# Kernel tuning notes

Measured on AMD Instinct MI355X. Metric: run time of the kernel, lower is better.

## Reference

```python
import jax, jax.numpy as jnp
import numpy as np

EPS = 1e-5

def _bn(x, w, b, rm, rv):
    # eval-mode BatchNorm over channel axis (x: [..., C] broadcastable)
    return (x - rm) * (w * jax.lax.rsqrt(rv + EPS)) + b

def setup_inputs() -> dict:
    key = jax.random.key(0)
    ks = jax.random.split(key, 20)
    B, C, H, W = 2, 64, 96, 96
    Cq = C // 8  # query/key channels
    Cr = C // 8  # SE reduction channels
    s = 0.05
    inp = {
        'x': jax.random.normal(ks[0], (B, C, H, W), jnp.float32),
        'wq': jax.random.normal(ks[1], (Cq, C), jnp.float32) * s,
        'bq': jnp.zeros((Cq,), jnp.float32),
        'wk': jax.random.normal(ks[2], (Cq, C), jnp.float32) * s,
        'bk': jnp.zeros((Cq,), jnp.float32),
        'wv': jax.random.normal(ks[3], (C, C), jnp.float32) * s,
        'bv': jnp.zeros((C,), jnp.float32),
        'gamma': jnp.full((1,), 0.5, jnp.float32),
        'bn_w': jnp.ones((C,), jnp.float32),
        'bn_b': jnp.zeros((C,), jnp.float32),
        'bn_rm': jax.random.normal(ks[4], (C,), jnp.float32) * 0.1,
        'bn_rv': jax.random.uniform(ks[5], (C,), jnp.float32) + 0.5,
        'se_w1': jax.random.normal(ks[6], (Cr, C), jnp.float32) * s,
        'se_b1': jnp.zeros((Cr,), jnp.float32),
        'se_bn1_w': jnp.ones((Cr,), jnp.float32),
        'se_bn1_b': jnp.zeros((Cr,), jnp.float32),
        'se_bn1_rm': jax.random.normal(ks[7], (Cr,), jnp.float32) * 0.1,
        'se_bn1_rv': jax.random.uniform(ks[8], (Cr,), jnp.float32) + 0.5,
        'se_w2': jax.random.normal(ks[9], (C, Cr), jnp.float32) * s,
        'se_b2': jnp.zeros((C,), jnp.float32),
        'se_bn2_w': jnp.ones((C,), jnp.float32),
        'se_bn2_b': jnp.zeros((C,), jnp.float32),
        'se_bn2_rm': jax.random.normal(ks[10], (C,), jnp.float32) * 0.1,
        'se_bn2_rv': jax.random.uniform(ks[11], (C,), jnp.float32) + 0.5,
    }
    return inp

def reference(x, wq, bq, wk, bk, wv, bv, gamma, bn_w, bn_b, bn_rm, bn_rv,
              se_w1, se_b1, se_bn1_w, se_bn1_b, se_bn1_rm, se_bn1_rv,
              se_w2, se_b2, se_bn2_w, se_bn2_b, se_bn2_rm, se_bn2_rv):
    B, C, H, W = x.shape
    N = H * W
    xf = x.reshape(B, C, N)
    # PAM branch: 1x1 conv projections
    q = jnp.einsum('oc,bcn->bno', wq, xf) + bq            # [B,N,C/8]
    k = jnp.einsum('oc,bcn->bon', wk, xf) + bk[:, None]    # [B,C/8,N]
    v = jnp.einsum('oc,bcn->bon', wv, xf) + bv[:, None]    # [B,C,N]
    energy = jnp.einsum('bno,bom->bnm', q, k)              # [B,N,N]
    attn = jax.nn.softmax(energy, axis=-1)
    # out[b,c,i] = sum_j v[b,c,j] * attn[b,i,j]  (bmm(V, attn^T))
    out = jnp.einsum('bcj,bij->bci', v, attn)
    out = gamma[0] * out
    out = _bn(out, bn_w[:, None], bn_b[:, None], bn_rm[:, None], bn_rv[:, None])
    pam = out.reshape(B, C, H, W)
    # SE branch: GAP + 1x1 conv-bn-relu x2, multiplicative gate
    a = xf.mean(axis=2)                                    # [B,C]
    a1 = jax.nn.relu(_bn(a @ se_w1.T + se_b1, se_bn1_w, se_bn1_b, se_bn1_rm, se_bn1_rv))
    a2 = jax.nn.relu(_bn(a1 @ se_w2.T + se_b2, se_bn2_w, se_bn2_b, se_bn2_rm, se_bn2_rv))
    se = x * a2[:, :, None, None]
    return x + se + pam
```

## Files before the change

### kernel.cpp

```cpp
#include <hip/hip_runtime.h>
#include <hip/hip_bf16.h>

#define B_SZ   2
#define C_CH   64
#define NQ     8
#define QKS    16
#define NPIX   9216
#define NKS    576
#define QBLKS  288
#define KPART  4
#define KEYS_P 2304
#define NCHUNK 36
#define SM_F   2080
#define NP4    2304
#define KSTEP2 1024
#define VSTEP  4096

typedef short bf16x8 __attribute__((ext_vector_type(8)));
typedef float f32x4  __attribute__((ext_vector_type(4)));
typedef float f32x16 __attribute__((ext_vector_type(16)));
typedef unsigned u32x4 __attribute__((ext_vector_type(4)));
typedef unsigned uint2v __attribute__((ext_vector_type(2)));

static __device__ __forceinline__ unsigned pack2bf(float a, float b){
    unsigned r;
    asm("v_cvt_pk_bf16_f32 %0, %1, %2" : "=v"(r) : "v"(a), "v"(b));
    return r;
}

static __device__ __forceinline__ float exp2r(float x){
    return __builtin_amdgcn_exp2f(x);
}

__global__ __launch_bounds__(256) void prep_kernel(
    const float* __restrict__ x,
    const float* __restrict__ wq, const float* __restrict__ bq,
    const float* __restrict__ wk, const float* __restrict__ bk,
    const float* __restrict__ wv, const float* __restrict__ bv,
    __hip_bfloat16* __restrict__ qp, __hip_bfloat16* __restrict__ kp,
    __hip_bfloat16* __restrict__ vswz, float* __restrict__ amean)
{
    const int blk = blockIdx.x, tid = threadIdx.x;
    if (blk < 144){
        int t  = blk*256 + tid;
        int n  = (t % NP4) * 4;
        int c8 = (t / NP4) & 7;
        int b  = t / (NP4*8);
        c8 = __builtin_amdgcn_readfirstlane(c8);
        b  = __builtin_amdgcn_readfirstlane(b);
        float acc[8][4];
#pragma unroll
        for (int k = 0; k < 8; ++k){
            float bvv = bv[c8*8 + k];
            acc[k][0] = bvv; acc[k][1] = bvv; acc[k][2] = bvv; acc[k][3] = bvv;
        }
#pragma unroll 4
        for (int ci = 0; ci < C_CH; ++ci){
            const float4 xv = *reinterpret_cast<const float4*>(
                x + (size_t)(b*C_CH + ci)*NPIX + n);
#pragma unroll
            for (int k = 0; k < 8; ++k){
                float w = wv[(c8*8 + k)*C_CH + ci];
                acc[k][0] = fmaf(xv.x, w, acc[k][0]);
                acc[k][1] = fmaf(xv.y, w, acc[k][1]);
                acc[k][2] = fmaf(xv.z, w, acc[k][2]);
                acc[k][3] = fmaf(xv.w, w, acc[k][3]);
            }
        }
#pragma unroll
        for (int k = 0; k < 8; ++k){
            int c = c8*8 + k;
            size_t base = ((size_t)((b*NKS + (n >> 4))*2 + (c >> 5)))*512
                        + (((n >> 3) & 1) << 8) + ((c & 31) << 3) + (n & 7);
            unsigned long long wpk =
                (unsigned long long)pack2bf(acc[k][0], acc[k][1]) |
                ((unsigned long long)pack2bf(acc[k][2], acc[k][3]) << 32);
            *reinterpret_cast<unsigned long long*>(vswz + base) = wpk;
        }
    } else if (blk < 180){
        int t  = (blk - 144)*256 + tid;
        int n  = (t % NP4) * 4;
        int o8 = (t / NP4) & 1;
        int b  = t / (NP4*2);
        o8 = __builtin_amdgcn_readfirstlane(o8);
        b  = __builtin_amdgcn_readfirstlane(b);
        const bool isq = (o8 == 0);
        const float* w    = isq ? wq : wk;
        const float* bias = isq ? bq : bk;
        float acc[8][4];
#pragma unroll
        for (int k = 0; k < 8; ++k){
            float bb = bias[k];
            acc[k][0] = bb; acc[k][1] = bb; acc[k][2] = bb; acc[k][3] = bb;
        }
#pragma unroll 4
        for (int ci = 0; ci < C_CH; ++ci){
            const float4 xv = *reinterpret_cast<const float4*>(
                x + (size_t)(b*C_CH + ci)*NPIX + n);
#pragma unroll
            for (int k = 0; k < 8; ++k){
                float wv_ = w[k*C_CH + ci];
                acc[k][0] = fmaf(xv.x, wv_, acc[k][0]);
                acc[k][1] = fmaf(xv.y, wv_, acc[k][1]);
                acc[k][2] = fmaf(xv.z, wv_, acc[k][2]);
                acc[k][3] = fmaf(xv.w, wv_, acc[k][3]);
            }
        }
        if (isq){
#pragma unroll
            for (int k = 0; k < 8; ++k)
#pragma unroll
                for (int px = 0; px < 4; ++px) acc[k][px] *= 1.44269504f;
        }
        __hip_bfloat16* dst = isq ? qp : kp;
        u32x4 zr; zr[0] = 0; zr[1] = 0; zr[2] = 0; zr[3] = 0;
#pragma unroll
        for (int px = 0; px < 4; ++px){
            u32x4 row;
            row[0] = pack2bf(acc[0][px], acc[1][px]);
            row[1] = pack2bf(acc[2][px], acc[3][px]);
            row[2] = pack2bf(acc[4][px], acc[5][px]);
            row[3] = pack2bf(acc[6][px], acc[7][px]);
            __hip_bfloat16* d0 = dst + ((size_t)(b*NPIX + n + px))*QKS;
            *reinterpret_cast<u32x4*>(d0)     = row;
            *reinterpret_cast<u32x4*>(d0 + 8) = zr;
        }
    } else {
        int bc = blk - 180;
        float s = 0.f;
        for (int i = tid; i < NPIX; i += 256) s += x[(size_t)bc*NPIX + i];
#pragma unroll
        for (int o = 32; o > 0; o >>= 1) s += __shfl_down(s, o, 64);
        __shared__ float red[4];
        if ((tid & 63) == 0) red[tid >> 6] = s;
        __syncthreads();
        if (tid == 0) amean[bc] = (red[0] + red[1] + red[2] + red[3]) * (1.f / (float)NPIX);
    }
}

__global__ __launch_bounds__(256, 4) void flash_fused(
    const __hip_bfloat16* __restrict__ qp,
    const __hip_bfloat16* __restrict__ kp,
    const __hip_bfloat16* __restrict__ vswz,
    const float* __restrict__ amean,
    const float* __restrict__ sw1, const float* __restrict__ sb1,
    const float* __restrict__ s1w, const float* __restrict__ s1b,
    const float* __restrict__ s1m, const float* __restrict__ s1v,
    const float* __restrict__ sw2, const float* __restrict__ sb2,
    const float* __restrict__ s2w, const float* __restrict__ s2b,
    const float* __restrict__ s2m, const float* __restrict__ s2v,
    const float* __restrict__ x,
    const float* __restrict__ gamma,
    const float* __restrict__ bnw, const float* __restrict__ bnb,
    const float* __restrict__ bnm, const float* __restrict__ bnv,
    float* __restrict__ out)
{
    __shared__ __align__(16) float sm[4*SM_F];

    const int qt2 = blockIdx.x, b = blockIdx.y;
    const int p  = threadIdx.x >> 6;
    const int l  = threadIdx.x & 63;
    const int lc = l & 31;
    const int lh = l >> 5;

    bf16x8 qfrag = *reinterpret_cast<const bf16x8*>(
        qp + ((size_t)(b*NPIX + qt2*32 + lc))*QKS + lh*8);

    bf16x8 ones;
#pragma unroll
    for (int i = 0; i < 8; ++i) ones[i] = (short)0x3F80;

    f32x16 zero16;
#pragma unroll
    for (int i = 0; i < 16; ++i) zero16[i] = 0.f;

    f32x16 Of0 = zero16, Of1 = zero16;
    f32x16 Lacc = zero16;

    const __hip_bfloat16* kptr = kp + ((size_t)(b*NPIX + p*KEYS_P + lc))*QKS + lh*8;
    const __hip_bfloat16* vptr = vswz + ((size_t)((b*NKS + p*(KEYS_P/16))*2))*512 + l*8;

    auto CHUNK = [&](const bf16x8& k0, const bf16x8& k1){
        bf16x8 vf[8];
#pragma unroll
        for (int t = 0; t < 8; ++t)
            vf[t] = *reinterpret_cast<const bf16x8*>(vptr + t*512);
        vptr += VSTEP;

        unsigned D[16];
#pragma unroll
        for (int kt = 0; kt < 2; ++kt){
            f32x16 s = __builtin_amdgcn_mfma_f32_32x32x16_bf16(
                kt ? k1 : k0, qfrag, zero16, 0, 0, 0);
#pragma unroll
            for (int g = 0; g < 4; ++g){
                float e0 = exp2r(s[4*g+0]), e1 = exp2r(s[4*g+1]);
                float e2 = exp2r(s[4*g+2]), e3 = exp2r(s[4*g+3]);
                D[kt*8 + g*2 + 0] = pack2bf(e0, e1);
                D[kt*8 + g*2 + 1] = pack2bf(e2, e3);
            }
        }
#pragma unroll
        for (int ks = 0; ks < 4; ++ks){
            const int base = (ks >> 1)*8 + (ks & 1)*4;
            uint2v r0 = __builtin_amdgcn_permlane32_swap(D[base+0], D[base+2], false, false);
            uint2v r1 = __builtin_amdgcn_permlane32_swap(D[base+1], D[base+3], false, false);
            u32x4 pu; pu[0] = r0[0]; pu[1] = r1[0]; pu[2] = r0[1]; pu[3] = r1[1];
            bf16x8 pf = __builtin_bit_cast(bf16x8, pu);
            Of0  = __builtin_amdgcn_mfma_f32_32x32x16_bf16(vf[ks*2+0], pf, Of0, 0, 0, 0);
            Of1  = __builtin_amdgcn_mfma_f32_32x32x16_bf16(vf[ks*2+1], pf, Of1, 0, 0, 0);
            Lacc = __builtin_amdgcn_mfma_f32_32x32x16_bf16(ones,       pf, Lacc, 0, 0, 0);
        }
    };

    bf16x8 kA0 = *reinterpret_cast<const bf16x8*>(kptr);
    bf16x8 kA1 = *reinterpret_cast<const bf16x8*>(kptr + 512);
    kptr += KSTEP2;
    bf16x8 kB0, kB1;
    for (int it = 0; it < (NCHUNK - 2)/2; ++it){
        kB0 = *reinterpret_cast<const bf16x8*>(kptr);
        kB1 = *reinterpret_cast<const bf16x8*>(kptr + 512);
        kptr += KSTEP2;
        CHUNK(kA0, kA1);
        kA0 = *reinterpret_cast<const bf16x8*>(kptr);
        kA1 = *reinterpret_cast<const bf16x8*>(kptr + 512);
        kptr += KSTEP2;
        CHUNK(kB0, kB1);
    }
    kB0 = *reinterpret_cast<const bf16x8*>(kptr);
    kB1 = *reinterpret_cast<const bf16x8*>(kptr + 512);
    CHUNK(kA0, kA1);
    CHUNK(kB0, kB1);

    float a1r;
    {
        int r8 = l & 7;
        float s = sb1[r8];
#pragma unroll 8
        for (int c = 0; c < C_CH; ++c)
            s = fmaf(amean[b*C_CH + c], sw1[r8*C_CH + c], s);
        s = (s - s1m[r8]) * (s1w[r8] * rsqrtf(s1v[r8] + 1e-5f)) + s1b[r8];
        a1r = fmaxf(s, 0.f);
    }

#pragma unroll
    for (int r = 0; r < 16; ++r){
        sm[p*SM_F +        r*64 + l] = Of0[r];
        sm[p*SM_F + 1024 + r*64 + l] = Of1[r];
    }
    if (l < 32) sm[p*SM_F + 2048 + l] = Lacc[0];
    __syncthreads();

    {
        const int i   = lc;
        const int cgs = p*2 + lh;
        float gam = gamma[0];

        float a1g[8];
#pragma unroll
        for (int j = 0; j < 8; ++j) a1g[j] = __shfl(a1r, (l & 56) | j, 64);

        float L = 0.f;
#pragma unroll
        for (int q = 0; q < 4; ++q) L += sm[q*SM_F + 2048 + i];
        float invL = 1.f / L;
        int n = qt2*32 + i;
#pragma unroll
        for (int r = 0; r < 8; ++r){
            int c = cgs*8 + r;
            float s = sb2[c];
#pragma unroll
            for (int j = 0; j < 8; ++j) s = fmaf(a1g[j], sw2[c*NQ + j], s);
            s = (s - s2m[c]) * (s2w[c] * rsqrtf(s2v[c] + 1e-5f)) + s2b[c];
            float a2v = fmaxf(s, 0.f);

            int c5   = c & 31;
            int reg  = (c5 & 3) + 4*(c5 >> 3);
            int lsrc = (c5 >> 2) & 1;
            int o    = (c >> 5)*1024 + reg*64 + lsrc*32 + i;
            float O = 0.f;
#pragma unroll
            for (int q = 0; q < 4; ++q) O += sm[q*SM_F + o];
            float pam = gam * O * invL;
            pam = (pam - bnm[c]) * (bnw[c] * rsqrtf(bnv[c] + 1e-5f)) + bnb[c];
            float xv = x[(size_t)(b*C_CH + c)*NPIX + n];
            out[(size_t)(b*C_CH + c)*NPIX + n] = fmaf(xv, a2v, xv + pam);
        }
    }
}

extern "C" void kernel_launch(void* const* d_in, const int* in_sizes, int n_in,
                              void* d_out, int out_size, void* d_ws, size_t ws_size,
                              hipStream_t stream)
{
    const float* x     = (const float*)d_in[0];
    const float* wq    = (const float*)d_in[1];
    const float* bq    = (const float*)d_in[2];
    const float* wk    = (const float*)d_in[3];
    const float* bk    = (const float*)d_in[4];
    const float* wv    = (const float*)d_in[5];
    const float* bv    = (const float*)d_in[6];
    const float* gamma = (const float*)d_in[7];
    const float* bnw   = (const float*)d_in[8];
    const float* bnb   = (const float*)d_in[9];
    const float* bnm   = (const float*)d_in[10];
    const float* bnv   = (const float*)d_in[11];
    const float* sw1   = (const float*)d_in[12];
    const float* sb1   = (const float*)d_in[13];
    const float* s1w   = (const float*)d_in[14];
    const float* s1b   = (const float*)d_in[15];
    const float* s1m   = (const float*)d_in[16];
    const float* s1v   = (const float*)d_in[17];
    const float* sw2   = (const float*)d_in[18];
    const float* sb2   = (const float*)d_in[19];
    const float* s2w   = (const float*)d_in[20];
    const float* s2b   = (const float*)d_in[21];
    const float* s2m   = (const float*)d_in[22];
    const float* s2v   = (const float*)d_in[23];

    size_t off = 0;
    auto give = [&](size_t bytes) -> void* {
        void* r = (char*)d_ws + off;
        off += (bytes + 255) & ~(size_t)255;
        return r;
    };
    __hip_bfloat16* qp   = (__hip_bfloat16*)give((size_t)B_SZ*NPIX*QKS*2);
    __hip_bfloat16* kp   = (__hip_bfloat16*)give((size_t)B_SZ*NPIX*QKS*2);
    __hip_bfloat16* vswz = (__hip_bfloat16*)give((size_t)B_SZ*C_CH*NPIX*2);
    float* amean = (float*)give((size_t)B_SZ*C_CH*4);

    prep_kernel<<<dim3(308), dim3(256), 0, stream>>>(x, wq, bq, wk, bk, wv, bv,
                                                     qp, kp, vswz, amean);
    flash_fused<<<dim3(QBLKS, B_SZ), dim3(256), 0, stream>>>(
        qp, kp, vswz, amean,
        sw1, sb1, s1w, s1b, s1m, s1v,
        sw2, sb2, s2w, s2b, s2m, s2v,
        x, gamma, bnw, bnb, bnm, bnv, (float*)d_out);
}
```

Measured before the change: 171.4 us.

## Double-buffer V fragments, add MFMA priority, halve LDS reduction buffer

The V fragment loads now join the K loads in a one-chunk-ahead double-buffered software pipeline, so global loads overlap the MFMA work of the previous chunk. The PV MFMA section is wrapped in s_setprio to favour matrix issue. The cross-wave reduction now uses a two-stage add into half-size shared memory, and the min-occupancy launch bound is dropped. Holding two sets of V registers raises VGPR pressure, which together with the removed launch bound may lower occupancy.

```diff
diff --git a/kernel.cpp b/kernel.cpp
--- a/kernel.cpp
+++ b/kernel.cpp
@@ -138,7 +138,7 @@
     }
 }
 
-__global__ __launch_bounds__(256, 4) void flash_fused(
+__global__ __launch_bounds__(256) void flash_fused(
     const __hip_bfloat16* __restrict__ qp,
     const __hip_bfloat16* __restrict__ kp,
     const __hip_bfloat16* __restrict__ vswz,
@@ -155,7 +155,7 @@
     const float* __restrict__ bnm, const float* __restrict__ bnv,
     float* __restrict__ out)
 {
-    __shared__ __align__(16) float sm[4*SM_F];
+    __shared__ __align__(16) float sm[2*SM_F];
 
     const int qt2 = blockIdx.x, b = blockIdx.y;
     const int p  = threadIdx.x >> 6;
@@ -180,13 +180,21 @@
     const __hip_bfloat16* kptr = kp + ((size_t)(b*NPIX + p*KEYS_P + lc))*QKS + lh*8;
     const __hip_bfloat16* vptr = vswz + ((size_t)((b*NKS + p*(KEYS_P/16))*2))*512 + l*8;
 
-    auto CHUNK = [&](const bf16x8& k0, const bf16x8& k1){
-        bf16x8 vf[8];
+    bf16x8 kA0, kA1, kB0, kB1;
+    bf16x8 vfA[8], vfB[8];
+
+    auto loadK = [&](bf16x8& d0, bf16x8& d1){
+        d0 = *reinterpret_cast<const bf16x8*>(kptr);
+        d1 = *reinterpret_cast<const bf16x8*>(kptr + 512);
+        kptr += KSTEP2;
+    };
+    auto loadV = [&](bf16x8 (&dst)[8]){
 #pragma unroll
         for (int t = 0; t < 8; ++t)
-            vf[t] = *reinterpret_cast<const bf16x8*>(vptr + t*512);
+            dst[t] = *reinterpret_cast<const bf16x8*>(vptr + t*512);
         vptr += VSTEP;
-
+    };
+    auto compute = [&](const bf16x8& k0, const bf16x8& k1, const bf16x8 (&vf)[8]){
         unsigned D[16];
 #pragma unroll
         for (int kt = 0; kt < 2; ++kt){
@@ -200,6 +208,7 @@
                 D[kt*8 + g*2 + 1] = pack2bf(e2, e3);
             }
         }
+        __builtin_amdgcn_s_setprio(1);
 #pragma unroll
         for (int ks = 0; ks < 4; ++ks){
             const int base = (ks >> 1)*8 + (ks & 1)*4;
@@ -211,26 +220,19 @@
             Of1  = __builtin_amdgcn_mfma_f32_32x32x16_bf16(vf[ks*2+1], pf, Of1, 0, 0, 0);
             Lacc = __builtin_amdgcn_mfma_f32_32x32x16_bf16(ones,       pf, Lacc, 0, 0, 0);
         }
+        __builtin_amdgcn_s_setprio(0);
     };
 
-    bf16x8 kA0 = *reinterpret_cast<const bf16x8*>(kptr);
-    bf16x8 kA1 = *reinterpret_cast<const bf16x8*>(kptr + 512);
-    kptr += KSTEP2;
-    bf16x8 kB0, kB1;
-    for (int it = 0; it < (NCHUNK - 2)/2; ++it){
-        kB0 = *reinterpret_cast<const bf16x8*>(kptr);
-        kB1 = *reinterpret_cast<const bf16x8*>(kptr + 512);
-        kptr += KSTEP2;
-        CHUNK(kA0, kA1);
-        kA0 = *reinterpret_cast<const bf16x8*>(kptr);
-        kA1 = *reinterpret_cast<const bf16x8*>(kptr + 512);
-        kptr += KSTEP2;
-        CHUNK(kB0, kB1);
-    }
-    kB0 = *reinterpret_cast<const bf16x8*>(kptr);
-    kB1 = *reinterpret_cast<const bf16x8*>(kptr + 512);
-    CHUNK(kA0, kA1);
-    CHUNK(kB0, kB1);
+    loadK(kA0, kA1); loadV(vfA);
+    for (int it = 0; it < 17; ++it){
+        loadK(kB0, kB1); loadV(vfB);
+        compute(kA0, kA1, vfA);
+        loadK(kA0, kA1); loadV(vfA);
+        compute(kB0, kB1, vfB);
+    }
+    loadK(kB0, kB1); loadV(vfB);
+    compute(kA0, kA1, vfA);
+    compute(kB0, kB1, vfB);
 
     float a1r;
     {
@@ -243,12 +245,24 @@
         a1r = fmaxf(s, 0.f);
     }
 
-#pragma unroll
-    for (int r = 0; r < 16; ++r){
-        sm[p*SM_F +        r*64 + l] = Of0[r];
-        sm[p*SM_F + 1024 + r*64 + l] = Of1[r];
-    }
-    if (l < 32) sm[p*SM_F + 2048 + l] = Lacc[0];
+    if (p >= 2){
+        const int ps = p - 2;
+#pragma unroll
+        for (int r = 0; r < 16; ++r){
+            sm[ps*SM_F +        r*64 + l] = Of0[r];
+            sm[ps*SM_F + 1024 + r*64 + l] = Of1[r];
+        }
+        if (l < 32) sm[ps*SM_F + 2048 + l] = Lacc[0];
+    }
+    __syncthreads();
+    if (p < 2){
+#pragma unroll
+        for (int r = 0; r < 16; ++r){
+            sm[p*SM_F +        r*64 + l] += Of0[r];
+            sm[p*SM_F + 1024 + r*64 + l] += Of1[r];
+        }
+        if (l < 32) sm[p*SM_F + 2048 + l] += Lacc[0];
+    }
     __syncthreads();
 
     {
@@ -260,9 +274,7 @@
 #pragma unroll
         for (int j = 0; j < 8; ++j) a1g[j] = __shfl(a1r, (l & 56) | j, 64);
 
-        float L = 0.f;
-#pragma unroll
-        for (int q = 0; q < 4; ++q) L += sm[q*SM_F + 2048 + i];
+        float L = sm[2048 + i] + sm[SM_F + 2048 + i];
         float invL = 1.f / L;
         int n = qt2*32 + i;
 #pragma unroll
@@ -278,9 +290,7 @@
             int reg  = (c5 & 3) + 4*(c5 >> 3);
             int lsrc = (c5 >> 2) & 1;
             int o    = (c >> 5)*1024 + reg*64 + lsrc*32 + i;
-            float O = 0.f;
-#pragma unroll
-            for (int q = 0; q < 4; ++q) O += sm[q*SM_F + o];
+            float O = sm[o] + sm[SM_F + o];
             float pam = gam * O * invL;
             pam = (pam - bnm[c]) * (bnw[c] * rsqrtf(bnv[c] + 1e-5f)) + bnb[c];
             float xv = x[(size_t)(b*C_CH + c)*NPIX + n];
```

After: 174.6 us. Within noise of the previous version (+1.9%).

## Split attention keys across grid z-dimension and add separate combine kernel

Applied to the files above, without the earlier changes.

The fused flash kernel now launches NSPLIT=4 blocks per query tile, each block processing a quarter of the keys (four waves, each handling 576 keys). Each block reduces its partial O and L sums in shared memory and writes them to a workspace. A new combine kernel sums the partials and applies the SE gating, BN and residual. The aim is to raise the block count from 576 to 2304 for better CU occupancy and a shorter per-block serial chain. In exchange it adds a kernel launch, plus roughly 19 MB of partial-result traffic written and then read back. It also adds s_setprio around the PV MFMA section and drops the occupancy hint from launch_bounds.

```diff
diff --git a/kernel.cpp b/kernel.cpp
--- a/kernel.cpp
+++ b/kernel.cpp
@@ -9,9 +9,11 @@
 #define NKS    576
 #define QBLKS  288
 #define KPART  4
-#define KEYS_P 2304
-#define NCHUNK 36
+#define NSPLIT 4
+#define KEYS_W 576
+#define NCHUNK_W 9
 #define SM_F   2080
+#define PSLOT  2080
 #define NP4    2304
 #define KSTEP2 1024
 #define VSTEP  4096
@@ -138,10 +140,123 @@
     }
 }
 
-__global__ __launch_bounds__(256, 4) void flash_fused(
+__global__ __launch_bounds__(256) void flash_fused(
     const __hip_bfloat16* __restrict__ qp,
     const __hip_bfloat16* __restrict__ kp,
     const __hip_bfloat16* __restrict__ vswz,
+    float* __restrict__ pws)
+{
+    __shared__ __align__(16) float sm[2*SM_F];
+
+    const int qt2 = blockIdx.x, b = blockIdx.y, z = blockIdx.z;
+    const int p  = threadIdx.x >> 6;
+    const int l  = threadIdx.x & 63;
+    const int lc = l & 31;
+    const int lh = l >> 5;
+
+    bf16x8 qfrag = *reinterpret_cast<const bf16x8*>(
+        qp + ((size_t)(b*NPIX + qt2*32 + lc))*QKS + lh*8);
+
+    bf16x8 ones;
+#pragma unroll
+    for (int i = 0; i < 8; ++i) ones[i] = (short)0x3F80;
+
+    f32x16 zero16;
+#pragma unroll
+    for (int i = 0; i < 16; ++i) zero16[i] = 0.f;
+
+    f32x16 Of0 = zero16, Of1 = zero16;
+    f32x16 Lacc = zero16;
+
+    const int kpart = z*KPART + p;
+    const __hip_bfloat16* kptr = kp + ((size_t)(b*NPIX + kpart*KEYS_W + lc))*QKS + lh*8;
+    const __hip_bfloat16* vptr = vswz + ((size_t)((b*NKS + kpart*(KEYS_W/16))*2))*512 + l*8;
+
+    auto CHUNK = [&](const bf16x8& k0, const bf16x8& k1){
+        bf16x8 vf[8];
+#pragma unroll
+        for (int t = 0; t < 8; ++t)
+            vf[t] = *reinterpret_cast<const bf16x8*>(vptr + t*512);
+        vptr += VSTEP;
+
+        unsigned D[16];
+#pragma unroll
+        for (int kt = 0; kt < 2; ++kt){
+            f32x16 s = __builtin_amdgcn_mfma_f32_32x32x16_bf16(
+                kt ? k1 : k0, qfrag, zero16, 0, 0, 0);
+#pragma unroll
+            for (int g = 0; g < 4; ++g){
+                float e0 = exp2r(s[4*g+0]), e1 = exp2r(s[4*g+1]);
+                float e2 = exp2r(s[4*g+2]), e3 = exp2r(s[4*g+3]);
+                D[kt*8 + g*2 + 0] = pack2bf(e0, e1);
+                D[kt*8 + g*2 + 1] = pack2bf(e2, e3);
+            }
+        }
+        __builtin_amdgcn_s_setprio(1);
+#pragma unroll
+        for (int ks = 0; ks < 4; ++ks){
+            const int base = (ks >> 1)*8 + (ks & 1)*4;
+            uint2v r0 = __builtin_amdgcn_permlane32_swap(D[base+0], D[base+2], false, false);
+            uint2v r1 = __builtin_amdgcn_permlane32_swap(D[base+1], D[base+3], false, false);
+            u32x4 pu; pu[0] = r0[0]; pu[1] = r1[0]; pu[2] = r0[1]; pu[3] = r1[1];
+            bf16x8 pf = __builtin_bit_cast(bf16x8, pu);
+            Of0  = __builtin_amdgcn_mfma_f32_32x32x16_bf16(vf[ks*2+0], pf, Of0, 0, 0, 0);
+            Of1  = __builtin_amdgcn_mfma_f32_32x32x16_bf16(vf[ks*2+1], pf, Of1, 0, 0, 0);
+            Lacc = __builtin_amdgcn_mfma_f32_32x32x16_bf16(ones,       pf, Lacc, 0, 0, 0);
+        }
+        __builtin_amdgcn_s_setprio(0);
+    };
+
+    bf16x8 kA0, kA1, kB0, kB1;
+    kA0 = *reinterpret_cast<const bf16x8*>(kptr);
+    kA1 = *reinterpret_cast<const bf16x8*>(kptr + 512);
+    kptr += KSTEP2;
+    for (int it = 0; it < 4; ++it){
+        kB0 = *reinterpret_cast<const bf16x8*>(kptr);
+        kB1 = *reinterpret_cast<const bf16x8*>(kptr + 512);
+        kptr += KSTEP2;
+        CHUNK(kA0, kA1);
+        if (it < 3){
+            kA0 = *reinterpret_cast<const bf16x8*>(kptr);
+            kA1 = *reinterpret_cast<const bf16x8*>(kptr + 512);
+            kptr += KSTEP2;
+        } else {
+            kA0 = *reinterpret_cast<const bf16x8*>(kptr);
+            kA1 = *reinterpret_cast<const bf16x8*>(kptr + 512);
+        }
+        CHUNK(kB0, kB1);
+    }
+    CHUNK(kA0, kA1);
+
+    if (p >= 2){
+        const int ps = p - 2;
+#pragma unroll
+        for (int r = 0; r < 16; ++r){
+            sm[ps*SM_F +        r*64 + l] = Of0[r];
+            sm[ps*SM_F + 1024 + r*64 + l] = Of1[r];
+        }
+        if (l < 32) sm[ps*SM_F + 2048 + l] = Lacc[0];
+    }
+    __syncthreads();
+    if (p < 2){
+#pragma unroll
+        for (int r = 0; r < 16; ++r){
+            sm[p*SM_F +        r*64 + l] += Of0[r];
+            sm[p*SM_F + 1024 + r*64 + l] += Of1[r];
+        }
+        if (l < 32) sm[p*SM_F + 2048 + l] += Lacc[0];
+    }
+    __syncthreads();
+
+    {
+        float* dst = pws + ((size_t)((b*QBLKS + qt2)*NSPLIT + z))*PSLOT;
+        for (int i = threadIdx.x; i < PSLOT; i += 256)
+            dst[i] = sm[i] + sm[SM_F + i];
+    }
+}
+
+__global__ __launch_bounds__(256) void combine_kernel(
+    const float* __restrict__ pws,
     const float* __restrict__ amean,
     const float* __restrict__ sw1, const float* __restrict__ sb1,
     const float* __restrict__ s1w, const float* __restrict__ s1b,
@@ -155,82 +270,11 @@
     const float* __restrict__ bnm, const float* __restrict__ bnv,
     float* __restrict__ out)
 {
-    __shared__ __align__(16) float sm[4*SM_F];
-
     const int qt2 = blockIdx.x, b = blockIdx.y;
     const int p  = threadIdx.x >> 6;
     const int l  = threadIdx.x & 63;
     const int lc = l & 31;
     const int lh = l >> 5;
-
-    bf16x8 qfrag = *reinterpret_cast<const bf16x8*>(
-        qp + ((size_t)(b*NPIX + qt2*32 + lc))*QKS + lh*8);
-
-    bf16x8 ones;
-#pragma unroll
-    for (int i = 0; i < 8; ++i) ones[i] = (short)0x3F80;
-
-    f32x16 zero16;
-#pragma unroll
-    for (int i = 0; i < 16; ++i) zero16[i] = 0.f;
-
-    f32x16 Of0 = zero16, Of1 = zero16;
-    f32x16 Lacc = zero16;
-
-    const __hip_bfloat16* kptr = kp + ((size_t)(b*NPIX + p*KEYS_P + lc))*QKS + lh*8;
-    const __hip_bfloat16* vptr = vswz + ((size_t)((b*NKS + p*(KEYS_P/16))*2))*512 + l*8;
-
-    auto CHUNK = [&](const bf16x8& k0, const bf16x8& k1){
-        bf16x8 vf[8];
-#pragma unroll
-        for (int t = 0; t < 8; ++t)
-            vf[t] = *reinterpret_cast<const bf16x8*>(vptr + t*512);
-        vptr += VSTEP;
-
-        unsigned D[16];
-#pragma unroll
-        for (int kt = 0; kt < 2; ++kt){
-            f32x16 s = __builtin_amdgcn_mfma_f32_32x32x16_bf16(
-                kt ? k1 : k0, qfrag, zero16, 0, 0, 0);
-#pragma unroll
-            for (int g = 0; g < 4; ++g){
-                float e0 = exp2r(s[4*g+0]), e1 = exp2r(s[4*g+1]);
-                float e2 = exp2r(s[4*g+2]), e3 = exp2r(s[4*g+3]);
-                D[kt*8 + g*2 + 0] = pack2bf(e0, e1);
-                D[kt*8 + g*2 + 1] = pack2bf(e2, e3);
-            }
-        }
-#pragma unroll
-        for (int ks = 0; ks < 4; ++ks){
-            const int base = (ks >> 1)*8 + (ks & 1)*4;
-            uint2v r0 = __builtin_amdgcn_permlane32_swap(D[base+0], D[base+2], false, false);
-            uint2v r1 = __builtin_amdgcn_permlane32_swap(D[base+1], D[base+3], false, false);
-            u32x4 pu; pu[0] = r0[0]; pu[1] = r1[0]; pu[2] = r0[1]; pu[3] = r1[1];
-            bf16x8 pf = __builtin_bit_cast(bf16x8, pu);
-            Of0  = __builtin_amdgcn_mfma_f32_32x32x16_bf16(vf[ks*2+0], pf, Of0, 0, 0, 0);
-            Of1  = __builtin_amdgcn_mfma_f32_32x32x16_bf16(vf[ks*2+1], pf, Of1, 0, 0, 0);
-            Lacc = __builtin_amdgcn_mfma_f32_32x32x16_bf16(ones,       pf, Lacc, 0, 0, 0);
-        }
-    };
-
-    bf16x8 kA0 = *reinterpret_cast<const bf16x8*>(kptr);
-    bf16x8 kA1 = *reinterpret_cast<const bf16x8*>(kptr + 512);
-    kptr += KSTEP2;
-    bf16x8 kB0, kB1;
-    for (int it = 0; it < (NCHUNK - 2)/2; ++it){
-        kB0 = *reinterpret_cast<const bf16x8*>(kptr);
-        kB1 = *reinterpret_cast<const bf16x8*>(kptr + 512);
-        kptr += KSTEP2;
-        CHUNK(kA0, kA1);
-        kA0 = *reinterpret_cast<const bf16x8*>(kptr);
-        kA1 = *reinterpret_cast<const bf16x8*>(kptr + 512);
-        kptr += KSTEP2;
-        CHUNK(kB0, kB1);
-    }
-    kB0 = *reinterpret_cast<const bf16x8*>(kptr);
-    kB1 = *reinterpret_cast<const bf16x8*>(kptr + 512);
-    CHUNK(kA0, kA1);
-    CHUNK(kB0, kB1);
 
     float a1r;
     {
@@ -243,49 +287,41 @@
         a1r = fmaxf(s, 0.f);
     }
 
-#pragma unroll
-    for (int r = 0; r < 16; ++r){
-        sm[p*SM_F +        r*64 + l] = Of0[r];
-        sm[p*SM_F + 1024 + r*64 + l] = Of1[r];
-    }
-    if (l < 32) sm[p*SM_F + 2048 + l] = Lacc[0];
-    __syncthreads();
-
-    {
-        const int i   = lc;
-        const int cgs = p*2 + lh;
-        float gam = gamma[0];
-
-        float a1g[8];
-#pragma unroll
-        for (int j = 0; j < 8; ++j) a1g[j] = __shfl(a1r, (l & 56) | j, 64);
-
-        float L = 0.f;
-#pragma unroll
-        for (int q = 0; q < 4; ++q) L += sm[q*SM_F + 2048 + i];
-        float invL = 1.f / L;
-        int n = qt2*32 + i;
-#pragma unroll
-        for (int r = 0; r < 8; ++r){
-            int c = cgs*8 + r;
-            float s = sb2[c];
-#pragma unroll
-            for (int j = 0; j < 8; ++j) s = fmaf(a1g[j], sw2[c*NQ + j], s);
-            s = (s - s2m[c]) * (s2w[c] * rsqrtf(s2v[c] + 1e-5f)) + s2b[c];
-            float a2v = fmaxf(s, 0.f);
-
-            int c5   = c & 31;
-            int reg  = (c5 & 3) + 4*(c5 >> 3);
-            int lsrc = (c5 >> 2) & 1;
-            int o    = (c >> 5)*1024 + reg*64 + lsrc*32 + i;
-            float O = 0.f;
-#pragma unroll
-            for (int q = 0; q < 4; ++q) O += sm[q*SM_F + o];
-            float pam = gam * O * invL;
-            pam = (pam - bnm[c]) * (bnw[c] * rsqrtf(bnv[c] + 1e-5f)) + bnb[c];
-            float xv = x[(size_t)(b*C_CH + c)*NPIX + n];
-            out[(size_t)(b*C_CH + c)*NPIX + n] = fmaf(xv, a2v, xv + pam);
-        }
+    const float* P0 = pws + ((size_t)((b*QBLKS + qt2)*NSPLIT))*PSLOT;
+
+    const int i   = lc;
+    const int cgs = p*2 + lh;
+    float gam = gamma[0];
+
+    float a1g[8];
+#pragma unroll
+    for (int j = 0; j < 8; ++j) a1g[j] = __shfl(a1r, (l & 56) | j, 64);
+
+    float L = 0.f;
+#pragma unroll
+    for (int zz = 0; zz < NSPLIT; ++zz) L += P0[zz*PSLOT + 2048 + i];
+    float invL = 1.f / L;
+    int n = qt2*32 + i;
+#pragma unroll
+    for (int r = 0; r < 8; ++r){
+        int c = cgs*8 + r;
+        float s = sb2[c];
+#pragma unroll
+        for (int j = 0; j < 8; ++j) s = fmaf(a1g[j], sw2[c*NQ + j], s);
+        s = (s - s2m[c]) * (s2w[c] * rsqrtf(s2v[c] + 1e-5f)) + s2b[c];
+        float a2v = fmaxf(s, 0.f);
+
+        int c5   = c & 31;
+        int reg  = (c5 & 3) + 4*(c5 >> 3);
+        int lsrc = (c5 >> 2) & 1;
+        int o    = (c >> 5)*1024 + reg*64 + lsrc*32 + i;
+        float O = 0.f;
+#pragma unroll
+        for (int zz = 0; zz < NSPLIT; ++zz) O += P0[zz*PSLOT + o];
+        float pam = gam * O * invL;
+        pam = (pam - bnm[c]) * (bnw[c] * rsqrtf(bnv[c] + 1e-5f)) + bnb[c];
+        float xv = x[(size_t)(b*C_CH + c)*NPIX + n];
+        out[(size_t)(b*C_CH + c)*NPIX + n] = fmaf(xv, a2v, xv + pam);
     }
 }
 
@@ -328,11 +364,13 @@
     __hip_bfloat16* kp   = (__hip_bfloat16*)give((size_t)B_SZ*NPIX*QKS*2);
     __hip_bfloat16* vswz = (__hip_bfloat16*)give((size_t)B_SZ*C_CH*NPIX*2);
     float* amean = (float*)give((size_t)B_SZ*C_CH*4);
+    float* pws   = (float*)give((size_t)B_SZ*QBLKS*NSPLIT*PSLOT*4);
 
     prep_kernel<<<dim3(308), dim3(256), 0, stream>>>(x, wq, bq, wk, bk, wv, bv,
                                                      qp, kp, vswz, amean);
-    flash_fused<<<dim3(QBLKS, B_SZ), dim3(256), 0, stream>>>(
-        qp, kp, vswz, amean,
+    flash_fused<<<dim3(QBLKS, B_SZ, NSPLIT), dim3(256), 0, stream>>>(qp, kp, vswz, pws);
+    combine_kernel<<<dim3(QBLKS, B_SZ), dim3(256), 0, stream>>>(
+        pws, amean,
         sw1, sb1, s1w, s1b, s1m, s1v,
         sw2, sb2, s2w, s2b, s2m, s2v,
         x, gamma, bnw, bnb, bnm, bnv, (float*)d_out);
```

New measurement: 171.5 us (median of 2 runs). Within noise of the previous version (+0.0%).
